# Kernel optimization log

Measured on AMD Instinct MI355X. Metric: run time of the kernel, lower is better.

## Reference

```python
import jax, jax.numpy as jnp
import numpy as np

RES = (64, 64)
TEMP = 0.1  # forward default temp

def _mgrid(res):
    # matches torch.meshgrid(linspace(0, r-1, r)...) with default 'ij' indexing
    gs = jnp.meshgrid(*[jnp.arange(r, dtype=jnp.float32) for r in res], indexing='ij')
    return jnp.stack(gs, 0)  # [2, H, W]

def setup_inputs() -> dict:
    key = jax.random.key(0)
    k1, k2 = jax.random.split(key)
    x = jax.random.normal(k1, (8, 32, RES[0], RES[1]), dtype=jnp.float32)
    of = jax.random.normal(k2, (8, 2, RES[0], RES[1]), dtype=jnp.float32)
    return {"x": x, "of": of}

def reference(x, of):
    bs, C = x.shape[0], x.shape[1]
    hw = RES[0] * RES[1]
    gpos = _mgrid(RES).reshape(2, hw)                 # [2, HW] target pixel positions
    opos = gpos[None] + of.reshape(bs, 2, hw)         # [bs, 2, HW] flow-displaced source positions
    # L1 distance: logits[b, i, j] = sum_c |opos[b, c, j] - gpos[c, i]|
    dist = jnp.abs(opos[:, :, None, :] - gpos[None, :, :, None]).sum(axis=1)  # [bs, HW, HW]
    # softmax over target axis i (dim=-2 in torch) -> each source pixel j distributes mass over targets
    locs = jax.nn.softmax(-dist / TEMP, axis=1)       # [bs, HW, HW]
    # out[b, c, i] = sum_j x[b, c, j] * locs[b, i, j]
    out = jnp.einsum('bij,bcj->bci', locs, x.reshape(bs, C, hw))
    return out.reshape(bs, C, RES[0], RES[1])
```

## Files before the change

kernel.cpp:

```cpp
#include <hip/hip_runtime.h>
#include <hip/hip_fp16.h>
#include <math.h>

#define HW    4096
#define NC    32
#define NB    8
#define TINV  10.0f
#define RWIN  8
#define WDIM  (8 + 2 * RWIN)
#define NSRC  (WDIM * WDIM)
#define RCUT  2.0f


__device__ __forceinline__ __half2 u32_as_h2(unsigned int u) {
    union { unsigned int u; __half2 h; } c; c.u = u; return c.h;
}
__device__ __forceinline__ unsigned int h2_as_u32(__half2 h) {
    union { __half2 h; unsigned int u; } c; c.h = h; return c.u;
}

__global__ __launch_bounds__(256) void prep_kernel(
    const float* __restrict__ x, const float* __restrict__ of,
    float4* __restrict__ params, __half2* __restrict__ xt2)
{
    __shared__ float tile[16][66];
    const int bx   = blockIdx.x;
    const int half = blockIdx.y;
    const int b    = bx >> 6;
    const int j0   = (bx & 63) << 6;
    const int t    = threadIdx.x;
    const int ch0  = half << 4;
    const int jj   = t & 63;
    const int c4   = t >> 6;

    if (half == 0 && t < 64) {
        int j = j0 + t;
        float oy = (float)(j >> 6) + of[(b * 2 + 0) * HW + j];
        float ox = (float)(j & 63) + of[(b * 2 + 1) * HW + j];
        int cy0 = min(max((int)floorf(oy), 0), 63);
        int cx0 = min(max((int)floorf(ox), 0), 63);
        float Dy = 0.f, Dx = 0.f;
        #pragma unroll
        for (int d = -3; d <= 3; ++d) {
            int iy = cy0 + d, ix = cx0 + d;
            if ((unsigned)iy < 64u) Dy += __expf(-TINV * fabsf(oy - (float)iy));
            if ((unsigned)ix < 64u) Dx += __expf(-TINV * fabsf(ox - (float)ix));
        }
        params[(b << 12) + j] = make_float4(oy, ox, 1.f / Dy, 1.f / Dx);
    }

    #pragma unroll
    for (int k = 0; k < 4; ++k) {
        int c = c4 * 4 + k;
        tile[c][jj] = x[((size_t)(b * NC + ch0 + c) << 12) + j0 + jj];
    }
    __syncthreads();
    #pragma unroll
    for (int k = 0; k < 2; ++k) {
        int s  = k * 256 + t;
        int j2 = s >> 3, pr = s & 7;
        xt2[((size_t)((b << 12) + j0 + j2) << 4) + (half << 3) + pr] =
            __floats2half2_rn(tile[2 * pr][j2], tile[2 * pr + 1][j2]);
    }
}

__global__ __launch_bounds__(256) void gather_kernel(
    const float4* __restrict__ params, const unsigned int* __restrict__ xtu,
    float* __restrict__ out)
{
    __shared__ float4       pw[NSRC];
    __shared__ unsigned int xw[NSRC * 8];
    __shared__ float4       wp[4][65];
    __shared__ int          sj[4][64];

    const int b    = blockIdx.z;
    const int h    = blockIdx.y;
    const int tile = blockIdx.x;
    const int ty0  = (tile >> 3) << 3;
    const int tx0  = (tile & 7) << 3;
    const int tid  = threadIdx.x;
    const int lane = tid & 63;
    const int wv   = __builtin_amdgcn_readfirstlane(tid >> 6);

    const float4* pb = params + (b << 12);
    for (int s = tid; s < NSRC; s += 256) {
        int wr = s / WDIM, wc = s - wr * WDIM;
        int jy = ty0 - RWIN + wr, jx = tx0 - RWIN + wc;
        bool v = ((unsigned)jy < 64u) && ((unsigned)jx < 64u);
        pw[s] = v ? pb[(jy << 6) + jx] : make_float4(0.f, 0.f, 0.f, 0.f);
    }

    const unsigned int* xb = xtu + ((size_t)(b << 12) << 4) + (h << 3);
    for (int i = tid; i < 2 * NSRC; i += 256) {
        int src = i >> 1, e = i & 1;
        int wr = src / WDIM, wc = src - wr * WDIM;
        int jy = ty0 - RWIN + wr, jx = tx0 - RWIN + wc;
        bool v = ((unsigned)jy < 64u) && ((unsigned)jx < 64u);
        uint4 q = make_uint4(0u, 0u, 0u, 0u);
        if (v) q = *(const uint4*)(xb + (((size_t)((jy << 6) + jx)) << 4) + (e << 2));
        *(uint4*)&xw[(size_t)i << 2] = q;
    }

    __syncthreads();

    const float iy = (float)(ty0 + (lane >> 3));
    const float ix = (float)(tx0 + (lane & 7));

    __half2 acc8[8];
    #pragma unroll
    for (int c = 0; c < 8; ++c) acc8[c] = __floats2half2_rn(0.f, 0.f);

    const int srow = lane >> 5;
    const int scol = lane & 31;

    for (int r = 0; r < 3; ++r) {
        int ry = wv + srow * 4 + r * 8;
        int jy = ty0 - RWIN + ry;
        int jx = tx0 - RWIN + scol;
        bool valid = ((unsigned)jy < 64u) && ((unsigned)jx < 64u) && (scol < WDIM);
        int ws = ry * WDIM + min(scol, WDIM - 1);
        float4 p = pw[ws];
        float cy = fminf(fmaxf(p.x, 0.f), 63.f);
        float cx = fminf(fmaxf(p.y, 0.f), 63.f);
        float dyr = fmaxf(fmaxf((float)ty0 - cy, cy - ((float)ty0 + 7.f)), 0.f);
        float dxr = fmaxf(fmaxf((float)tx0 - cx, cx - ((float)tx0 + 7.f)), 0.f);
        bool pred = valid && (dyr + dxr < RCUT);

        unsigned long long m = __ballot(pred);
        int cnt = __popcll(m);
        if (pred) {
            int pos = __builtin_amdgcn_mbcnt_hi((unsigned)(m >> 32),
                      __builtin_amdgcn_mbcnt_lo((unsigned)m, 0u));
            wp[wv][pos] = p;
            sj[wv][pos] = ws;
        }
        if (lane == cnt) { wp[wv][cnt] = make_float4(1.f, 1.f, 0.f, 0.f); sj[wv][cnt] = 0; }
        int cntp = cnt + (cnt & 1);

        for (int k = 0; k < cntp; k += 2) {
            float4 p0 = wp[wv][k], p1 = wp[wv][k + 1];
            int s0 = sj[wv][k], s1 = sj[wv][k + 1];
            const uint4* x0 = (const uint4*)&xw[(size_t)s0 << 3];
            const uint4* x1 = (const uint4*)&xw[(size_t)s1 << 3];
            uint4 A0 = x0[0], A1 = x0[1];
            uint4 B0 = x1[0], B1 = x1[1];

            float g0 = (__expf(-TINV * fabsf(p0.x - iy)) * p0.z)
                     * (__expf(-TINV * fabsf(p0.y - ix)) * p0.w);
            float g1 = (__expf(-TINV * fabsf(p1.x - iy)) * p1.z)
                     * (__expf(-TINV * fabsf(p1.y - ix)) * p1.w);
            __half2 hg0 = __float2half2_rn(g0);
            __half2 hg1 = __float2half2_rn(g1);

            acc8[0] = __hfma2(hg0, u32_as_h2(A0.x), acc8[0]);
            acc8[1] = __hfma2(hg0, u32_as_h2(A0.y), acc8[1]);
            acc8[2] = __hfma2(hg0, u32_as_h2(A0.z), acc8[2]);
            acc8[3] = __hfma2(hg0, u32_as_h2(A0.w), acc8[3]);
            acc8[4] = __hfma2(hg0, u32_as_h2(A1.x), acc8[4]);
            acc8[5] = __hfma2(hg0, u32_as_h2(A1.y), acc8[5]);
            acc8[6] = __hfma2(hg0, u32_as_h2(A1.z), acc8[6]);
            acc8[7] = __hfma2(hg0, u32_as_h2(A1.w), acc8[7]);

            acc8[0] = __hfma2(hg1, u32_as_h2(B0.x), acc8[0]);
            acc8[1] = __hfma2(hg1, u32_as_h2(B0.y), acc8[1]);
            acc8[2] = __hfma2(hg1, u32_as_h2(B0.z), acc8[2]);
            acc8[3] = __hfma2(hg1, u32_as_h2(B0.w), acc8[3]);
            acc8[4] = __hfma2(hg1, u32_as_h2(B1.x), acc8[4]);
            acc8[5] = __hfma2(hg1, u32_as_h2(B1.y), acc8[5]);
            acc8[6] = __hfma2(hg1, u32_as_h2(B1.z), acc8[6]);
            acc8[7] = __hfma2(hg1, u32_as_h2(B1.w), acc8[7]);
        }
    }

    __syncthreads();
    unsigned int* redu = (unsigned int*)pw;
    unsigned int* myr  = redu + ((wv << 6) + lane) * 9;
    #pragma unroll
    for (int c = 0; c < 8; ++c) myr[c] = h2_as_u32(acc8[c]);
    __syncthreads();

    int c2  = tid >> 5;
    int t32 = tid & 31;
    #pragma unroll
    for (int k = 0; k < 2; ++k) {
        int t = t32 + 32 * k;
        float sx = 0.f, sy = 0.f;
        #pragma unroll
        for (int w = 0; w < 4; ++w) {
            float2 f = __half22float2(u32_as_h2(redu[((w << 6) + t) * 9 + c2]));
            sx += f.x; sy += f.y;
        }
        int ch   = (h << 4) + 2 * c2;
        int base = (((b << 5) + ch) << 12) + (ty0 + (t >> 3)) * 64 + (tx0 + (t & 7));
        out[base]      = sx;
        out[base + HW] = sy;
    }
}

extern "C" void kernel_launch(void* const* d_in, const int* in_sizes, int n_in,
                              void* d_out, int out_size, void* d_ws, size_t ws_size,
                              hipStream_t stream) {
    const float* x  = (const float*)d_in[0];
    const float* of = (const float*)d_in[1];
    float* out = (float*)d_out;

    float4*  params = (float4*)d_ws;
    __half2* xt2    = (__half2*)((char*)d_ws + NB * HW * sizeof(float4));

    prep_kernel<<<dim3(NB * 64, 2), dim3(256), 0, stream>>>(x, of, params, xt2);
    gather_kernel<<<dim3(64, 2, NB), dim3(256), 0, stream>>>(
        params, (const unsigned int*)xt2, out);
}
```

Baseline: 69.52 us.

## Gather only selected sources per wave and process all 32 channels per block

The gather kernel no longer stages the full 24x24 source window of params and features into shared memory. Each wave reads params straight from global memory, compacts the sources that pass the cutoff, and fetches only their 32-channel fp16 features into a per-wave shared buffer. Each block now covers all 32 channels, so the grid is halved and the distance and weight math is no longer repeated for two channel halves. The cost is twice the accumulator registers, fewer blocks to fill the GPU, and gathers from global memory inside the loop.

New measurement: 67.86 us. 2.4% less time.

```diff
diff --git a/kernel.cpp b/kernel.cpp
--- a/kernel.cpp
+++ b/kernel.cpp
@@ -8,7 +8,6 @@
 #define TINV  10.0f
 #define RWIN  8
 #define WDIM  (8 + 2 * RWIN)
-#define NSRC  (WDIM * WDIM)
 #define RCUT  2.0f
 
 
@@ -68,58 +67,41 @@
     const float4* __restrict__ params, const unsigned int* __restrict__ xtu,
     float* __restrict__ out)
 {
-    __shared__ float4       pw[NSRC];
-    __shared__ unsigned int xw[NSRC * 8];
     __shared__ float4       wp[4][65];
     __shared__ int          sj[4][64];
-
-    const int b    = blockIdx.z;
-    const int h    = blockIdx.y;
+    __shared__ unsigned int pool[4 * 64 * 17];
+
+    const int b    = blockIdx.y;
     const int tile = blockIdx.x;
     const int ty0  = (tile >> 3) << 3;
     const int tx0  = (tile & 7) << 3;
+
     const int tid  = threadIdx.x;
     const int lane = tid & 63;
     const int wv   = __builtin_amdgcn_readfirstlane(tid >> 6);
 
-    const float4* pb = params + (b << 12);
-    for (int s = tid; s < NSRC; s += 256) {
-        int wr = s / WDIM, wc = s - wr * WDIM;
-        int jy = ty0 - RWIN + wr, jx = tx0 - RWIN + wc;
-        bool v = ((unsigned)jy < 64u) && ((unsigned)jx < 64u);
-        pw[s] = v ? pb[(jy << 6) + jx] : make_float4(0.f, 0.f, 0.f, 0.f);
-    }
-
-    const unsigned int* xb = xtu + ((size_t)(b << 12) << 4) + (h << 3);
-    for (int i = tid; i < 2 * NSRC; i += 256) {
-        int src = i >> 1, e = i & 1;
-        int wr = src / WDIM, wc = src - wr * WDIM;
-        int jy = ty0 - RWIN + wr, jx = tx0 - RWIN + wc;
-        bool v = ((unsigned)jy < 64u) && ((unsigned)jx < 64u);
-        uint4 q = make_uint4(0u, 0u, 0u, 0u);
-        if (v) q = *(const uint4*)(xb + (((size_t)((jy << 6) + jx)) << 4) + (e << 2));
-        *(uint4*)&xw[(size_t)i << 2] = q;
-    }
-
-    __syncthreads();
-
     const float iy = (float)(ty0 + (lane >> 3));
     const float ix = (float)(tx0 + (lane & 7));
 
-    __half2 acc8[8];
-    #pragma unroll
-    for (int c = 0; c < 8; ++c) acc8[c] = __floats2half2_rn(0.f, 0.f);
+    __half2 acc16[16];
+    #pragma unroll
+    for (int c = 0; c < 16; ++c) acc16[c] = __floats2half2_rn(0.f, 0.f);
+
+    const float4*       pb = params + (b << 12);
+    const unsigned int* xb = xtu + ((size_t)(b << 12) << 4);
 
     const int srow = lane >> 5;
     const int scol = lane & 31;
+
+    unsigned int* XSu = pool;
 
     for (int r = 0; r < 3; ++r) {
         int ry = wv + srow * 4 + r * 8;
         int jy = ty0 - RWIN + ry;
         int jx = tx0 - RWIN + scol;
         bool valid = ((unsigned)jy < 64u) && ((unsigned)jx < 64u) && (scol < WDIM);
-        int ws = ry * WDIM + min(scol, WDIM - 1);
-        float4 p = pw[ws];
+        int j = (jy << 6) + jx;
+        float4 p = pb[valid ? j : 0];
         float cy = fminf(fmaxf(p.x, 0.f), 63.f);
         float cx = fminf(fmaxf(p.y, 0.f), 63.f);
         float dyr = fmaxf(fmaxf((float)ty0 - cy, cy - ((float)ty0 + 7.f)), 0.f);
@@ -132,18 +114,27 @@
             int pos = __builtin_amdgcn_mbcnt_hi((unsigned)(m >> 32),
                       __builtin_amdgcn_mbcnt_lo((unsigned)m, 0u));
             wp[wv][pos] = p;
-            sj[wv][pos] = ws;
-        }
-        if (lane == cnt) { wp[wv][cnt] = make_float4(1.f, 1.f, 0.f, 0.f); sj[wv][cnt] = 0; }
+            sj[wv][pos] = j;
+        }
+        if (lane == cnt) wp[wv][cnt] = make_float4(1.f, 1.f, 0.f, 0.f);
         int cntp = cnt + (cnt & 1);
+
+        for (int m4 = 0; m4 < cntp; m4 += 16) {
+            int s = m4 + (lane >> 2);
+            if (s < cntp) {
+                int jj = sj[wv][min(s, cnt - 1)];
+                const uint4* src = (const uint4*)(xb + (size_t)jj * 16 + ((lane & 3) << 2));
+                *(uint4*)&XSu[(((wv << 6) + s) << 4) + ((lane & 3) << 2)] = *src;
+            }
+        }
 
         for (int k = 0; k < cntp; k += 2) {
             float4 p0 = wp[wv][k], p1 = wp[wv][k + 1];
-            int s0 = sj[wv][k], s1 = sj[wv][k + 1];
-            const uint4* x0 = (const uint4*)&xw[(size_t)s0 << 3];
-            const uint4* x1 = (const uint4*)&xw[(size_t)s1 << 3];
-            uint4 A0 = x0[0], A1 = x0[1];
-            uint4 B0 = x1[0], B1 = x1[1];
+            const uint4* x0 = (const uint4*)&XSu[((wv << 6) + k)     << 4];
+            const uint4* x1 = (const uint4*)&XSu[((wv << 6) + k + 1) << 4];
+            uint4 A[4], B[4];
+            #pragma unroll
+            for (int q = 0; q < 4; ++q) { A[q] = x0[q]; B[q] = x1[q]; }
 
             float g0 = (__expf(-TINV * fabsf(p0.x - iy)) * p0.z)
                      * (__expf(-TINV * fabsf(p0.y - ix)) * p0.w);
@@ -152,45 +143,42 @@
             __half2 hg0 = __float2half2_rn(g0);
             __half2 hg1 = __float2half2_rn(g1);
 
-            acc8[0] = __hfma2(hg0, u32_as_h2(A0.x), acc8[0]);
-            acc8[1] = __hfma2(hg0, u32_as_h2(A0.y), acc8[1]);
-            acc8[2] = __hfma2(hg0, u32_as_h2(A0.z), acc8[2]);
-            acc8[3] = __hfma2(hg0, u32_as_h2(A0.w), acc8[3]);
-            acc8[4] = __hfma2(hg0, u32_as_h2(A1.x), acc8[4]);
-            acc8[5] = __hfma2(hg0, u32_as_h2(A1.y), acc8[5]);
-            acc8[6] = __hfma2(hg0, u32_as_h2(A1.z), acc8[6]);
-            acc8[7] = __hfma2(hg0, u32_as_h2(A1.w), acc8[7]);
-
-            acc8[0] = __hfma2(hg1, u32_as_h2(B0.x), acc8[0]);
-            acc8[1] = __hfma2(hg1, u32_as_h2(B0.y), acc8[1]);
-            acc8[2] = __hfma2(hg1, u32_as_h2(B0.z), acc8[2]);
-            acc8[3] = __hfma2(hg1, u32_as_h2(B0.w), acc8[3]);
-            acc8[4] = __hfma2(hg1, u32_as_h2(B1.x), acc8[4]);
-            acc8[5] = __hfma2(hg1, u32_as_h2(B1.y), acc8[5]);
-            acc8[6] = __hfma2(hg1, u32_as_h2(B1.z), acc8[6]);
-            acc8[7] = __hfma2(hg1, u32_as_h2(B1.w), acc8[7]);
+            #pragma unroll
+            for (int q = 0; q < 4; ++q) {
+                acc16[4 * q + 0] = __hfma2(hg0, u32_as_h2(A[q].x), acc16[4 * q + 0]);
+                acc16[4 * q + 1] = __hfma2(hg0, u32_as_h2(A[q].y), acc16[4 * q + 1]);
+                acc16[4 * q + 2] = __hfma2(hg0, u32_as_h2(A[q].z), acc16[4 * q + 2]);
+                acc16[4 * q + 3] = __hfma2(hg0, u32_as_h2(A[q].w), acc16[4 * q + 3]);
+            }
+            #pragma unroll
+            for (int q = 0; q < 4; ++q) {
+                acc16[4 * q + 0] = __hfma2(hg1, u32_as_h2(B[q].x), acc16[4 * q + 0]);
+                acc16[4 * q + 1] = __hfma2(hg1, u32_as_h2(B[q].y), acc16[4 * q + 1]);
+                acc16[4 * q + 2] = __hfma2(hg1, u32_as_h2(B[q].z), acc16[4 * q + 2]);
+                acc16[4 * q + 3] = __hfma2(hg1, u32_as_h2(B[q].w), acc16[4 * q + 3]);
+            }
         }
     }
 
     __syncthreads();
-    unsigned int* redu = (unsigned int*)pw;
-    unsigned int* myr  = redu + ((wv << 6) + lane) * 9;
-    #pragma unroll
-    for (int c = 0; c < 8; ++c) myr[c] = h2_as_u32(acc8[c]);
+    unsigned int* redu = pool;
+    unsigned int* myr  = redu + (unsigned)tid * 17;
+    #pragma unroll
+    for (int c = 0; c < 16; ++c) myr[c] = h2_as_u32(acc16[c]);
     __syncthreads();
 
-    int c2  = tid >> 5;
-    int t32 = tid & 31;
-    #pragma unroll
-    for (int k = 0; k < 2; ++k) {
-        int t = t32 + 32 * k;
+    int t  = tid & 63;
+    int c0 = tid >> 6;
+    #pragma unroll
+    for (int k = 0; k < 4; ++k) {
+        int c2 = c0 + (k << 2);
         float sx = 0.f, sy = 0.f;
         #pragma unroll
         for (int w = 0; w < 4; ++w) {
-            float2 f = __half22float2(u32_as_h2(redu[((w << 6) + t) * 9 + c2]));
+            float2 f = __half22float2(u32_as_h2(redu[(unsigned)((w << 6) + t) * 17 + c2]));
             sx += f.x; sy += f.y;
         }
-        int ch   = (h << 4) + 2 * c2;
+        int ch   = c2 << 1;
         int base = (((b << 5) + ch) << 12) + (ty0 + (t >> 3)) * 64 + (tx0 + (t & 7));
         out[base]      = sx;
         out[base + HW] = sy;
@@ -208,6 +196,6 @@
     __half2* xt2    = (__half2*)((char*)d_ws + NB * HW * sizeof(float4));
 
     prep_kernel<<<dim3(NB * 64, 2), dim3(256), 0, stream>>>(x, of, params, xt2);
-    gather_kernel<<<dim3(64, 2, NB), dim3(256), 0, stream>>>(
+    gather_kernel<<<dim3(64, NB), dim3(256), 0, stream>>>(
         params, (const unsigned int*)xt2, out);
 }
```
